# Optimization experiments

Measured on AMD Instinct MI355X. Metric: run time of the kernel, lower is better.

## Reference

```python
import jax, jax.numpy as jnp
import numpy as np

HIDDEN = 2048
GAMMA = 0.96875
SCALE_BASE = 512  # XPOS default from torchscale / Jamie-Stirling/RetNet


def _xpos(x, downscale=False):
    # x: [B, L, d]. Faithful port of XPOS with offset=0.
    B, L, d = x.shape
    half = d // 2
    # per-dim scale vector: (arange(0,d,2) + 0.4d) / (1.4d)
    scale_vec = (jnp.arange(0, d, 2, dtype=jnp.float32) + 0.4 * d) / (1.4 * d)  # [half]
    power = jnp.arange(L, dtype=jnp.float32) / SCALE_BASE                        # [L]
    scale = scale_vec[None, :] ** power[:, None]                                 # [L, half]
    # fixed_pos_embedding over `half` frequency dims
    inv_freq = 1.0 / (10000.0 ** (jnp.arange(half, dtype=jnp.float32) / half))   # [half]
    sinusoid = jnp.arange(L, dtype=jnp.float32)[:, None] * inv_freq[None, :]     # [L, half]
    sin, cos = jnp.sin(sinusoid), jnp.cos(sinusoid)
    if downscale:
        scale = 1.0 / scale
    # duplicate_interleave: [L, half] -> [L, d] with each column repeated twice
    sin_s = jnp.repeat(sin * scale, 2, axis=-1)  # [L, d]
    cos_s = jnp.repeat(cos * scale, 2, axis=-1)  # [L, d]
    # rotate_every_two
    x1 = x[..., 0::2]
    x2 = x[..., 1::2]
    rot = jnp.stack((-x2, x1), axis=-1).reshape(x.shape)
    return x * cos_s[None] + rot * sin_s[None]


def _decay_matrix(L):
    n = jnp.arange(L)[:, None]
    m = jnp.arange(L)[None, :]
    mask = n >= m
    # clamp exponent to avoid overflow where masked (torch sets NaN->0)
    D = jnp.where(mask, GAMMA ** jnp.maximum(n - m, 0).astype(jnp.float32), 0.0)
    return D  # [L, L]


def setup_inputs() -> dict:
    key = jax.random.key(0)
    kx, kq, kk, kv = jax.random.split(key, 4)
    B, S, H = 4, 2048, HIDDEN
    X = jax.random.normal(kx, (B, S, H), dtype=jnp.float32)
    W_Q = jax.random.normal(kq, (H, H), dtype=jnp.float32) / H
    W_K = jax.random.normal(kk, (H, H), dtype=jnp.float32) / H
    W_V = jax.random.normal(kv, (H, H), dtype=jnp.float32) / H
    return {"X": X, "W_Q": W_Q, "W_K": W_K, "W_V": W_V}


def reference(X, W_Q, W_K, W_V):
    B, S, H = X.shape
    Q = _xpos(X @ W_Q)                   # [B, S, H]
    K = _xpos(X @ W_K, downscale=True)   # [B, S, H]
    V = X @ W_V                          # [B, S, H]
    D = _decay_matrix(S)                 # [S, S]
    att = jnp.einsum("bnh,bmh->bnm", Q, K) * D[None]  # [B, S, S]
    return att @ V                       # [B, S, H]
```

## Files before the change

### kernel.cpp

```cpp
#include <hip/hip_runtime.h>
#include <math.h>


typedef __attribute__((ext_vector_type(8))) short short8;
typedef __attribute__((ext_vector_type(4))) float f32x4;
typedef __attribute__((ext_vector_type(4))) unsigned short us4;

#define BM 128
#define BN 128
#define BK 64

static __device__ __forceinline__ unsigned short f2bf(float f) {
    unsigned int u = __float_as_uint(f);
    u += 0x7FFFu + ((u >> 16) & 1u);
    return (unsigned short)(u >> 16);
}

static __device__ __forceinline__ void gload16(const unsigned short* g, unsigned short* l) {
    __builtin_amdgcn_global_load_lds(
        (const __attribute__((address_space(1))) unsigned int*)g,
        (__attribute__((address_space(3))) unsigned int*)l, 16, 0, 0);
}

template <int STAGE>
__global__ __launch_bounds__(256)
void gemm_bt(const unsigned short* __restrict__ A,
             const unsigned short* __restrict__ Bt,
             void* __restrict__ Cv,
             unsigned short* __restrict__ Cq,
             unsigned short* __restrict__ Ck,
             unsigned short* __restrict__ Cvt,
             int lda, int ldb, int Kd,
             long long sA, long long sB, long long sC)
{
    constexpr int S = 2048, H = 2048;
    const int rowBase = blockIdx.y * BM;
    const int colBase = blockIdx.x * BN;

    if (STAGE == 3 && blockIdx.x > blockIdx.y) {
        unsigned short* att = (unsigned short*)Cv + (long long)blockIdx.z * sC;
        int r = threadIdx.x >> 1, c = (threadIdx.x & 1) * 64;
        unsigned short* p = att + (size_t)(rowBase + r) * S + colBase + c;
        uint4 z = make_uint4(0, 0, 0, 0);
#pragma unroll
        for (int q = 0; q < 8; ++q) ((uint4*)p)[q] = z;
        return;
    }

    A  += (long long)blockIdx.z * sA;
    Bt += (long long)blockIdx.z * sB;

    __shared__ unsigned short As[BM * BK];
    __shared__ unsigned short Bs[BN * BK];

    const int tid  = threadIdx.x;
    const int wave = tid >> 6;
    const int lane = tid & 63;
    const int wm = (wave & 1) * 64;
    const int wn = (wave >> 1) * 64;

    f32x4 acc[4][4];
#pragma unroll
    for (int i = 0; i < 4; ++i)
#pragma unroll
        for (int j = 0; j < 4; ++j) acc[i][j] = (f32x4){0.f, 0.f, 0.f, 0.f};

    int kmax = Kd;
    if (STAGE == 4) { int km = colBase + BN; kmax = km < Kd ? km : Kd; }

    const int srow = wave * 32 + (lane >> 3);
    const int schunk = ((lane & 7) ^ ((lane >> 3) & 7)) * 8;
    const unsigned short* ga = A  + (size_t)(rowBase + srow) * lda + schunk;
    const unsigned short* gb = Bt + (size_t)(colBase + srow) * ldb + schunk;
    unsigned short* lA = As + wave * 2048;
    unsigned short* lB = Bs + wave * 2048;

#pragma unroll
    for (int q = 0; q < 4; ++q) {
        gload16(ga + (size_t)q * 8 * lda, lA + q * 512);
        gload16(gb + (size_t)q * 8 * ldb, lB + q * 512);
    }

    const int fr = lane & 15;
    const int qd = lane >> 4;
    const int fsw = fr & 7;

    for (int k0 = 0; k0 < kmax; k0 += BK) {
        __syncthreads();
        short8 af0[4], bf0[4], af1[4], bf1[4];
#pragma unroll
        for (int i = 0; i < 4; ++i) {
            int row = wm + i * 16 + fr;
            af0[i] = *(const short8*)&As[row * 64 + ((qd ^ fsw) * 8)];
            af1[i] = *(const short8*)&As[row * 64 + (((4 + qd) ^ fsw) * 8)];
        }
#pragma unroll
        for (int j = 0; j < 4; ++j) {
            int row = wn + j * 16 + fr;
            bf0[j] = *(const short8*)&Bs[row * 64 + ((qd ^ fsw) * 8)];
            bf1[j] = *(const short8*)&Bs[row * 64 + (((4 + qd) ^ fsw) * 8)];
        }
        __syncthreads();
        if (k0 + BK < kmax) {
            const unsigned short* ga2 = ga + k0 + BK;
            const unsigned short* gb2 = gb + k0 + BK;
#pragma unroll
            for (int q = 0; q < 4; ++q) {
                gload16(ga2 + (size_t)q * 8 * lda, lA + q * 512);
                gload16(gb2 + (size_t)q * 8 * ldb, lB + q * 512);
            }
        }
#pragma unroll
        for (int i = 0; i < 4; ++i)
#pragma unroll
            for (int j = 0; j < 4; ++j)
                acc[i][j] = __builtin_amdgcn_mfma_f32_16x16x32_bf16(af0[i], bf0[j], acc[i][j], 0, 0, 0);
#pragma unroll
        for (int i = 0; i < 4; ++i)
#pragma unroll
            for (int j = 0; j < 4; ++j)
                acc[i][j] = __builtin_amdgcn_mfma_f32_16x16x32_bf16(af1[i], bf1[j], acc[i][j], 0, 0, 0);
    }

    if (STAGE == 1) {
        const int mode = colBase >> 11;
        if (mode < 2) {
            unsigned short* Co = (mode == 0) ? Cq : Ck;
            const float psgn = (mode == 1) ? -1.953125e-3f : 1.953125e-3f;
#pragma unroll
            for (int j = 0; j < 4; ++j) {
                int gc = (colBase & 2047) + wn + j * 16 + fr;
                float c0 = (float)(gc & ~1);
                float l2sv = log2f((c0 + 819.2f) * (1.0f / 2867.2f)) * psgn;
                float invf = exp2f(c0 * -0.0064881407f);
                float s1, c1;
                sincosf(invf, &s1, &c1);
#pragma unroll
                for (int i = 0; i < 4; ++i) {
                    int gr0 = rowBase + wm + i * 16 + qd * 4;
                    float fn = (float)(gr0 & (S - 1));
                    float sN, cN;
                    sincosf(fn * invf, &sN, &cN);
#pragma unroll
                    for (int r = 0; r < 4; ++r) {
                        float scale = exp2f(fn * l2sv);
                        float cs = cN * scale, ss = sN * scale;
                        float v = acc[i][j][r];
                        float o = __shfl_xor(v, 1);
                        float res = (gc & 1) ? fmaf(v, cs, o * ss) : fmaf(v, cs, -o * ss);
                        Co[(size_t)(gr0 + r) * H + gc] = f2bf(res);
                        float sn2 = sN * c1 + cN * s1;
                        cN = cN * c1 - sN * s1;
                        sN = sn2;
                        fn += 1.0f;
                    }
                }
            }
        } else {
#pragma unroll
            for (int j = 0; j < 4; ++j) {
                int gh = (colBase & 2047) + wn + j * 16 + fr;
#pragma unroll
                for (int i = 0; i < 4; ++i) {
                    int gm0 = rowBase + wm + i * 16 + qd * 4;
                    us4 p;
#pragma unroll
                    for (int r = 0; r < 4; ++r) p[r] = f2bf(acc[i][j][r]);
                    *(us4*)&Cvt[(size_t)gh * 8192 + gm0] = p;
                }
            }
        }
    } else if (STAGE == 3) {
        unsigned short* att = (unsigned short*)Cv + (long long)blockIdx.z * sC;
#pragma unroll
        for (int j = 0; j < 4; ++j) {
            int m = colBase + wn + j * 16 + fr;
#pragma unroll
            for (int i = 0; i < 4; ++i) {
                int n0 = rowBase + wm + i * 16 + qd * 4;
#pragma unroll
                for (int r = 0; r < 4; ++r) {
                    int d = n0 + r - m;
                    float v = (d >= 0) ? acc[i][j][r] * exp2f((float)d * -0.045803598f) : 0.0f;
                    att[(size_t)(n0 + r) * S + m] = f2bf(v);
                }
            }
        }
    } else {
        float* Co = (float*)Cv + (long long)blockIdx.z * sC;
#pragma unroll
        for (int j = 0; j < 4; ++j) {
            int gn = colBase + wn + j * 16 + fr;
#pragma unroll
            for (int i = 0; i < 4; ++i) {
                int gh0 = rowBase + wm + i * 16 + qd * 4;
                *(f32x4*)&Co[(size_t)gn * H + gh0] = acc[i][j];
            }
        }
    }
}

__global__ __launch_bounds__(256)
void cvt_f32_bf16(const float* __restrict__ x, unsigned short* __restrict__ y) {
    int i = blockIdx.x * 256 + threadIdx.x;
    float4 v = ((const float4*)x)[i];
    us4 o = {f2bf(v.x), f2bf(v.y), f2bf(v.z), f2bf(v.w)};
    ((us4*)y)[i] = o;
}

__global__ __launch_bounds__(256)
void cvt_transpose3(const float* __restrict__ W0, const float* __restrict__ W1,
                    const float* __restrict__ W2, unsigned short* __restrict__ Wt) {
    __shared__ float t[64][65];
    const float* W = (blockIdx.z == 0) ? W0 : (blockIdx.z == 1) ? W1 : W2;
    unsigned short* Wo = Wt + (size_t)blockIdx.z * 4194304;
    int bx = blockIdx.x * 64, by = blockIdx.y * 64;
    int tx = threadIdx.x & 63, ty = threadIdx.x >> 6;
#pragma unroll
    for (int r = 0; r < 64; r += 4)
        t[ty + r][tx] = W[(size_t)(by + ty + r) * 2048 + bx + tx];
    __syncthreads();
#pragma unroll
    for (int r = 0; r < 64; r += 4)
        Wo[(size_t)(bx + ty + r) * 2048 + by + tx] = f2bf(t[tx][ty + r]);
}

extern "C" void kernel_launch(void* const* d_in, const int* in_sizes, int n_in,
                              void* d_out, int out_size, void* d_ws, size_t ws_size,
                              hipStream_t stream) {
    const int S = 2048, H = 2048;
    const long long MH = 16777216;
    const long long HH = 4194304;
    const long long SH = (long long)S * H;
    const long long SS = (long long)S * S;

    const float* X  = (const float*)d_in[0];
    const float* WQ = (const float*)d_in[1];
    const float* WK = (const float*)d_in[2];
    const float* WV = (const float*)d_in[3];
    float* out = (float*)d_out;

    unsigned short* Xb    = (unsigned short*)d_ws;
    unsigned short* WtAll = Xb + MH;
    unsigned short* Qb    = WtAll + 3 * HH;
    unsigned short* Kb    = Qb + MH;
    unsigned short* Vt    = Kb + MH;
    unsigned short* att   = Vt + MH;

    cvt_f32_bf16<<<16384, 256, 0, stream>>>(X, Xb);
    cvt_transpose3<<<dim3(32, 32, 3), 256, 0, stream>>>(WQ, WK, WV, WtAll);

    gemm_bt<1><<<dim3(48, 64), 256, 0, stream>>>(Xb, WtAll, nullptr, Qb, Kb, Vt,
                                                 H, H, H, 0, 0, 0);
    gemm_bt<3><<<dim3(16, 16, 4), 256, 0, stream>>>(Qb, Kb, att, nullptr, nullptr, nullptr,
                                                    H, H, H, SH, SH, SS);
    gemm_bt<4><<<dim3(16, 16, 4), 256, 0, stream>>>(Vt, att, out, nullptr, nullptr, nullptr,
                                                    8192, S, S, S, SS, SH);
}
```

Before: 495.4 us.

## Enlarge GEMM tiles to 256x256 with double-buffered LDS and explicit waitcnt pipelining

All three GEMM stages now use 256x256 block tiles with 512 threads, where each wave computes a 128x64 sub-tile. The global-to-LDS loads are double-buffered, with the prefetch of the next K slice overlapped through manual vmcnt waits and raw barriers. The attention stage no longer zero-fills the upper-triangle tiles, because the final stage limits its K range to the causal rows. The final stage swaps operands so att is the A matrix, which turns its output into scalar strided stores. The changes aim to raise arithmetic intensity and hide load latency, at the cost of 128KB of LDS per block, lower occupancy, and fewer blocks (256 per batched GEMM) to fill the CUs.

```diff
diff --git a/kernel.cpp b/kernel.cpp
--- a/kernel.cpp
+++ b/kernel.cpp
@@ -6,8 +6,8 @@
 typedef __attribute__((ext_vector_type(4))) float f32x4;
 typedef __attribute__((ext_vector_type(4))) unsigned short us4;
 
-#define BM 128
-#define BN 128
+#define BM 256
+#define BN 256
 #define BK 64
 
 static __device__ __forceinline__ unsigned short f2bf(float f) {
@@ -23,7 +23,7 @@
 }
 
 template <int STAGE>
-__global__ __launch_bounds__(256)
+__global__ __launch_bounds__(512, 2)
 void gemm_bt(const unsigned short* __restrict__ A,
              const unsigned short* __restrict__ Bt,
              void* __restrict__ Cv,
@@ -37,89 +37,92 @@
     const int rowBase = blockIdx.y * BM;
     const int colBase = blockIdx.x * BN;
 
-    if (STAGE == 3 && blockIdx.x > blockIdx.y) {
-        unsigned short* att = (unsigned short*)Cv + (long long)blockIdx.z * sC;
-        int r = threadIdx.x >> 1, c = (threadIdx.x & 1) * 64;
-        unsigned short* p = att + (size_t)(rowBase + r) * S + colBase + c;
-        uint4 z = make_uint4(0, 0, 0, 0);
-#pragma unroll
-        for (int q = 0; q < 8; ++q) ((uint4*)p)[q] = z;
-        return;
-    }
+    if (STAGE == 3 && blockIdx.x > blockIdx.y) return;
 
     A  += (long long)blockIdx.z * sA;
     Bt += (long long)blockIdx.z * sB;
 
-    __shared__ unsigned short As[BM * BK];
-    __shared__ unsigned short Bs[BN * BK];
+    __shared__ unsigned short As[2 * BM * BK];
+    __shared__ unsigned short Bs[2 * BN * BK];
 
     const int tid  = threadIdx.x;
     const int wave = tid >> 6;
     const int lane = tid & 63;
-    const int wm = (wave & 1) * 64;
-    const int wn = (wave >> 1) * 64;
-
-    f32x4 acc[4][4];
-#pragma unroll
-    for (int i = 0; i < 4; ++i)
+    const int wm = (wave >> 2) * 128;
+    const int wn = (wave & 3) * 64;
+
+    f32x4 acc[8][4];
+#pragma unroll
+    for (int i = 0; i < 8; ++i)
 #pragma unroll
         for (int j = 0; j < 4; ++j) acc[i][j] = (f32x4){0.f, 0.f, 0.f, 0.f};
 
     int kmax = Kd;
-    if (STAGE == 4) { int km = colBase + BN; kmax = km < Kd ? km : Kd; }
+    if (STAGE == 4) kmax = rowBase + BM;
 
     const int srow = wave * 32 + (lane >> 3);
     const int schunk = ((lane & 7) ^ ((lane >> 3) & 7)) * 8;
     const unsigned short* ga = A  + (size_t)(rowBase + srow) * lda + schunk;
     const unsigned short* gb = Bt + (size_t)(colBase + srow) * ldb + schunk;
-    unsigned short* lA = As + wave * 2048;
-    unsigned short* lB = Bs + wave * 2048;
-
-#pragma unroll
-    for (int q = 0; q < 4; ++q) {
-        gload16(ga + (size_t)q * 8 * lda, lA + q * 512);
-        gload16(gb + (size_t)q * 8 * ldb, lB + q * 512);
+    unsigned short* lA0 = As + wave * 2048;
+    unsigned short* lB0 = Bs + wave * 2048;
+
+    const int fr  = lane & 15;
+    const int qd  = lane >> 4;
+    const int fsw = fr & 7;
+    const int nt  = kmax >> 6;
+
+#pragma unroll
+    for (int g = 0; g < 4; ++g) {
+        gload16(ga + (size_t)g * 8 * lda, lA0 + g * 512);
+        gload16(gb + (size_t)g * 8 * ldb, lB0 + g * 512);
     }
 
-    const int fr = lane & 15;
-    const int qd = lane >> 4;
-    const int fsw = fr & 7;
-
-    for (int k0 = 0; k0 < kmax; k0 += BK) {
-        __syncthreads();
-        short8 af0[4], bf0[4], af1[4], bf1[4];
-#pragma unroll
-        for (int i = 0; i < 4; ++i) {
-            int row = wm + i * 16 + fr;
-            af0[i] = *(const short8*)&As[row * 64 + ((qd ^ fsw) * 8)];
-            af1[i] = *(const short8*)&As[row * 64 + (((4 + qd) ^ fsw) * 8)];
-        }
-#pragma unroll
-        for (int j = 0; j < 4; ++j) {
-            int row = wn + j * 16 + fr;
-            bf0[j] = *(const short8*)&Bs[row * 64 + ((qd ^ fsw) * 8)];
-            bf1[j] = *(const short8*)&Bs[row * 64 + (((4 + qd) ^ fsw) * 8)];
-        }
-        __syncthreads();
-        if (k0 + BK < kmax) {
-            const unsigned short* ga2 = ga + k0 + BK;
-            const unsigned short* gb2 = gb + k0 + BK;
-#pragma unroll
-            for (int q = 0; q < 4; ++q) {
-                gload16(ga2 + (size_t)q * 8 * lda, lA + q * 512);
-                gload16(gb2 + (size_t)q * 8 * ldb, lB + q * 512);
-            }
-        }
-#pragma unroll
-        for (int i = 0; i < 4; ++i)
-#pragma unroll
-            for (int j = 0; j < 4; ++j)
-                acc[i][j] = __builtin_amdgcn_mfma_f32_16x16x32_bf16(af0[i], bf0[j], acc[i][j], 0, 0, 0);
-#pragma unroll
-        for (int i = 0; i < 4; ++i)
-#pragma unroll
-            for (int j = 0; j < 4; ++j)
-                acc[i][j] = __builtin_amdgcn_mfma_f32_16x16x32_bf16(af1[i], bf1[j], acc[i][j], 0, 0, 0);
+    for (int t = 0; t < nt; ++t) {
+        const int b = t & 1;
+        if (t + 1 < nt) {
+            const unsigned short* gA = ga + (t + 1) * BK;
+            const unsigned short* gB = gb + (t + 1) * BK;
+            unsigned short* lA = lA0 + (b ^ 1) * 16384;
+            unsigned short* lB = lB0 + (b ^ 1) * 16384;
+#pragma unroll
+            for (int g = 0; g < 4; ++g) {
+                gload16(gA + (size_t)g * 8 * lda, lA + g * 512);
+                gload16(gB + (size_t)g * 8 * ldb, lB + g * 512);
+            }
+            __builtin_amdgcn_sched_barrier(0);
+            asm volatile("s_waitcnt vmcnt(8)" ::: "memory");
+        } else {
+            __builtin_amdgcn_sched_barrier(0);
+            asm volatile("s_waitcnt vmcnt(0)" ::: "memory");
+        }
+        __builtin_amdgcn_sched_barrier(0);
+        __builtin_amdgcn_s_barrier();
+        asm volatile("" ::: "memory");
+
+        const unsigned short* Ab = As + b * 16384;
+        const unsigned short* Bb = Bs + b * 16384;
+#pragma unroll
+        for (int kk = 0; kk < 2; ++kk) {
+            short8 bfr[4], afr[8];
+#pragma unroll
+            for (int j = 0; j < 4; ++j) {
+                int row = wn + j * 16 + fr;
+                bfr[j] = *(const short8*)&Bb[row * 64 + (((kk * 4 + qd) ^ fsw) * 8)];
+            }
+#pragma unroll
+            for (int i = 0; i < 8; ++i) {
+                int row = wm + i * 16 + fr;
+                afr[i] = *(const short8*)&Ab[row * 64 + (((kk * 4 + qd) ^ fsw) * 8)];
+            }
+#pragma unroll
+            for (int i = 0; i < 8; ++i)
+#pragma unroll
+                for (int j = 0; j < 4; ++j)
+                    acc[i][j] = __builtin_amdgcn_mfma_f32_16x16x32_bf16(afr[i], bfr[j], acc[i][j], 0, 0, 0);
+        }
+        asm volatile("" ::: "memory");
+        __builtin_amdgcn_s_barrier();
     }
 
     if (STAGE == 1) {
@@ -136,7 +139,7 @@
                 float s1, c1;
                 sincosf(invf, &s1, &c1);
 #pragma unroll
-                for (int i = 0; i < 4; ++i) {
+                for (int i = 0; i < 8; ++i) {
                     int gr0 = rowBase + wm + i * 16 + qd * 4;
                     float fn = (float)(gr0 & (S - 1));
                     float sN, cN;
@@ -161,7 +164,7 @@
             for (int j = 0; j < 4; ++j) {
                 int gh = (colBase & 2047) + wn + j * 16 + fr;
 #pragma unroll
-                for (int i = 0; i < 4; ++i) {
+                for (int i = 0; i < 8; ++i) {
                     int gm0 = rowBase + wm + i * 16 + qd * 4;
                     us4 p;
 #pragma unroll
@@ -176,7 +179,7 @@
         for (int j = 0; j < 4; ++j) {
             int m = colBase + wn + j * 16 + fr;
 #pragma unroll
-            for (int i = 0; i < 4; ++i) {
+            for (int i = 0; i < 8; ++i) {
                 int n0 = rowBase + wm + i * 16 + qd * 4;
 #pragma unroll
                 for (int r = 0; r < 4; ++r) {
@@ -190,11 +193,13 @@
         float* Co = (float*)Cv + (long long)blockIdx.z * sC;
 #pragma unroll
         for (int j = 0; j < 4; ++j) {
-            int gn = colBase + wn + j * 16 + fr;
-#pragma unroll
-            for (int i = 0; i < 4; ++i) {
-                int gh0 = rowBase + wm + i * 16 + qd * 4;
-                *(f32x4*)&Co[(size_t)gn * H + gh0] = acc[i][j];
+            int gh = colBase + wn + j * 16 + fr;
+#pragma unroll
+            for (int i = 0; i < 8; ++i) {
+                int gn0 = rowBase + wm + i * 16 + qd * 4;
+#pragma unroll
+                for (int r = 0; r < 4; ++r)
+                    Co[(size_t)(gn0 + r) * H + gh] = acc[i][j][r];
             }
         }
     }
@@ -250,10 +255,10 @@
     cvt_f32_bf16<<<16384, 256, 0, stream>>>(X, Xb);
     cvt_transpose3<<<dim3(32, 32, 3), 256, 0, stream>>>(WQ, WK, WV, WtAll);
 
-    gemm_bt<1><<<dim3(48, 64), 256, 0, stream>>>(Xb, WtAll, nullptr, Qb, Kb, Vt,
+    gemm_bt<1><<<dim3(24, 32), 512, 0, stream>>>(Xb, WtAll, nullptr, Qb, Kb, Vt,
                                                  H, H, H, 0, 0, 0);
-    gemm_bt<3><<<dim3(16, 16, 4), 256, 0, stream>>>(Qb, Kb, att, nullptr, nullptr, nullptr,
-                                                    H, H, H, SH, SH, SS);
-    gemm_bt<4><<<dim3(16, 16, 4), 256, 0, stream>>>(Vt, att, out, nullptr, nullptr, nullptr,
-                                                    8192, S, S, S, SS, SH);
-}
+    gemm_bt<3><<<dim3(8, 8, 4), 512, 0, stream>>>(Qb, Kb, att, nullptr, nullptr, nullptr,
+                                                  H, H, H, SH, SH, SS);
+    gemm_bt<4><<<dim3(8, 8, 4), 512, 0, stream>>>(att, Vt, out, nullptr, nullptr, nullptr,
+                                                  S, 8192, S, SS, 2048, SH);
+}
```

Measured after the change: 516.3 us. 1.04x slower.

## Swap operand roles in att@V GEMM, skip upper-triangle zeroing, swizzle projection blocks

Applied to the files above, without the earlier changes.

The final GEMM now passes att as the A operand and Vt as the B operand, so output rows come from attention rows and the causal k-limit is taken from rowBase. This allows scalar strided stores to out. Stage 3 no longer writes zeros into upper-triangular att tiles, since stage 4 never reads beyond the diagonal. The projection GEMM gets a block-index swizzle meant to improve L2 reuse. The trade-off is that output stores change from vectorized f32x4 writes to scalar column-strided writes, which may coalesce less well.

```diff
diff --git a/kernel.cpp b/kernel.cpp
--- a/kernel.cpp
+++ b/kernel.cpp
@@ -34,18 +34,18 @@
              long long sA, long long sB, long long sC)
 {
     constexpr int S = 2048, H = 2048;
-    const int rowBase = blockIdx.y * BM;
-    const int colBase = blockIdx.x * BN;
-
-    if (STAGE == 3 && blockIdx.x > blockIdx.y) {
-        unsigned short* att = (unsigned short*)Cv + (long long)blockIdx.z * sC;
-        int r = threadIdx.x >> 1, c = (threadIdx.x & 1) * 64;
-        unsigned short* p = att + (size_t)(rowBase + r) * S + colBase + c;
-        uint4 z = make_uint4(0, 0, 0, 0);
-#pragma unroll
-        for (int q = 0; q < 8; ++q) ((uint4*)p)[q] = z;
-        return;
-    }
+
+    if (STAGE == 3 && blockIdx.x > blockIdx.y) return;
+
+    int bx = blockIdx.x, by = blockIdx.y;
+    if (STAGE == 1) {
+        int bid = by * 48 + bx;
+        int sw  = (bid & 7) * 384 + (bid >> 3);
+        by = sw / 48;
+        bx = sw - by * 48;
+    }
+    const int rowBase = by * BM;
+    const int colBase = bx * BN;
 
     A  += (long long)blockIdx.z * sA;
     Bt += (long long)blockIdx.z * sB;
@@ -66,7 +66,7 @@
         for (int j = 0; j < 4; ++j) acc[i][j] = (f32x4){0.f, 0.f, 0.f, 0.f};
 
     int kmax = Kd;
-    if (STAGE == 4) { int km = colBase + BN; kmax = km < Kd ? km : Kd; }
+    if (STAGE == 4) { int km = rowBase + BM; kmax = km < Kd ? km : Kd; }
 
     const int srow = wave * 32 + (lane >> 3);
     const int schunk = ((lane & 7) ^ ((lane >> 3) & 7)) * 8;
@@ -190,11 +190,13 @@
         float* Co = (float*)Cv + (long long)blockIdx.z * sC;
 #pragma unroll
         for (int j = 0; j < 4; ++j) {
-            int gn = colBase + wn + j * 16 + fr;
+            int gh = colBase + wn + j * 16 + fr;
 #pragma unroll
             for (int i = 0; i < 4; ++i) {
-                int gh0 = rowBase + wm + i * 16 + qd * 4;
-                *(f32x4*)&Co[(size_t)gn * H + gh0] = acc[i][j];
+                int gn0 = rowBase + wm + i * 16 + qd * 4;
+#pragma unroll
+                for (int r = 0; r < 4; ++r)
+                    Co[(size_t)(gn0 + r) * H + gh] = acc[i][j][r];
             }
         }
     }
@@ -254,6 +256,6 @@
                                                  H, H, H, 0, 0, 0);
     gemm_bt<3><<<dim3(16, 16, 4), 256, 0, stream>>>(Qb, Kb, att, nullptr, nullptr, nullptr,
                                                     H, H, H, SH, SH, SS);
-    gemm_bt<4><<<dim3(16, 16, 4), 256, 0, stream>>>(Vt, att, out, nullptr, nullptr, nullptr,
-                                                    8192, S, S, S, SS, SH);
-}
+    gemm_bt<4><<<dim3(16, 16, 4), 256, 0, stream>>>(att, Vt, out, nullptr, nullptr, nullptr,
+                                                    S, 8192, S, SS, 2048, SH);
+}
```

After: 531.1 us. 7.2% more time.
